# Kernel tuning notes

Measured on AMD Instinct MI355X. Metric: run time of the kernel, lower is better.

Reference implementation:

```python
import jax, jax.numpy as jnp
import numpy as np

S, N, CM, CZ, H, C = 256, 512, 256, 128, 8, 32
EPS = 1e-5


def layer_norm(x, gamma, beta):
    mu = jnp.mean(x, axis=-1, keepdims=True)
    var = jnp.var(x, axis=-1, keepdims=True)
    return (x - mu) * jax.lax.rsqrt(var + EPS) * gamma + beta


def setup_inputs() -> dict:
    key = jax.random.key(0)
    ks = jax.random.split(key, 10)
    sc = lambda fan_in: 1.0 / np.sqrt(fan_in)
    return {
        "msa_rep": jax.random.normal(ks[0], (S, N, CM), dtype=jnp.float32),
        "pair_rep": jax.random.normal(ks[1], (N, N, CZ), dtype=jnp.float32),
        "ln_msa_g": jnp.ones((CM,), jnp.float32),
        "ln_msa_b": jnp.zeros((CM,), jnp.float32),
        "Wv": jax.random.uniform(ks[2], (CM, H * C), jnp.float32, -sc(CM), sc(CM)),
        "bv": jax.random.uniform(ks[3], (H * C,), jnp.float32, -sc(CM), sc(CM)),
        "ln_z_g": jnp.ones((CZ,), jnp.float32),
        "ln_z_b": jnp.zeros((CZ,), jnp.float32),
        "Wb": jax.random.uniform(ks[4], (CZ, H), jnp.float32, -sc(CZ), sc(CZ)),
        "bb": jax.random.uniform(ks[5], (H,), jnp.float32, -sc(CZ), sc(CZ)),
        "Wg": jax.random.uniform(ks[6], (CM, H * C), jnp.float32, -sc(CM), sc(CM)),
        "bg": jax.random.uniform(ks[7], (H * C,), jnp.float32, -sc(CM), sc(CM)),
        "Wp": jax.random.uniform(ks[8], (H * C, CM), jnp.float32, -sc(H * C), sc(H * C)),
    }


def reference(msa_rep, pair_rep, ln_msa_g, ln_msa_b, Wv, bv, ln_z_g, ln_z_b, Wb, bb, Wg, bg, Wp):
    m = layer_norm(msa_rep, ln_msa_g, ln_msa_b)                 # [S,N,CM]
    v = (m @ Wv + bv).reshape(S, N, H, C)                       # [S,N,H,C]
    g = jax.nn.sigmoid(m @ Wg + bg).reshape(S, N, H, C)         # [S,N,H,C]
    b = layer_norm(pair_rep, ln_z_g, ln_z_b) @ Wb + bb          # [N,N,H]
    w = jax.nn.softmax(b, axis=-2)                              # softmax over key residue j
    # o[s,i,h,c] = sum_j w[i,j,h] * v[s,j,h,c]
    o = g * jnp.einsum('ijh,sjhc->sihc', w, v)                  # [S,N,H,C]
    return o.reshape(S, N, H * C) @ Wp                          # [S,N,CM]
```

## Files before the change

kernel.cpp:

```cpp
#include <hip/hip_runtime.h>
#include <hip/hip_bf16.h>
#include <math.h>

#define S 256
#define N 512
#define CM 256
#define CZ 128
#define H 8
#define C 32
#define HC 256

typedef __attribute__((ext_vector_type(8))) short short8v;
typedef __attribute__((ext_vector_type(4))) float f32x4;

#define GLOBAL_LOAD_LDS16(gsrc, ldst)                                          \
  __builtin_amdgcn_global_load_lds(                                            \
      (const __attribute__((address_space(1))) void*)(gsrc),                   \
      (__attribute__((address_space(3))) void*)(ldst), 16, 0, 0)

__global__ __launch_bounds__(256) void k_prep(
    const float* __restrict__ Wv, const float* __restrict__ Wg, const float* __restrict__ Wp,
    __hip_bfloat16* __restrict__ Wcat_t, __hip_bfloat16* __restrict__ Wp_t)
{
  const int k = blockIdx.x;
  const int n = threadIdx.x;
  Wcat_t[(size_t)n * CM + k]        = __float2bfloat16(Wv[(size_t)k * HC + n]);
  Wcat_t[(size_t)(n + HC) * CM + k] = __float2bfloat16(Wg[(size_t)k * HC + n]);
  Wp_t[(size_t)n * CM + k]          = __float2bfloat16(Wp[(size_t)k * CM + n]);
}

__global__ __launch_bounds__(256) void k_ln(
    const float* __restrict__ msa, const float* __restrict__ gamma, const float* __restrict__ beta,
    __hip_bfloat16* __restrict__ mbf)
{
  const int t = threadIdx.x, wav = t >> 6, lane = t & 63;
  const size_t row = (size_t)blockIdx.x * 4 + wav;
  const int k0 = lane * 4;
  const float4 xv = *(const float4*)(msa + row * CM + k0);
  float s  = xv.x + xv.y + xv.z + xv.w;
  float s2 = xv.x * xv.x + xv.y * xv.y + xv.z * xv.z + xv.w * xv.w;
#pragma unroll
  for (int off = 32; off > 0; off >>= 1) {
    s  += __shfl_xor(s, off);
    s2 += __shfl_xor(s2, off);
  }
  const float mu = s * (1.f / CM);
  const float rstd = rsqrtf(s2 * (1.f / CM) - mu * mu + 1e-5f);
  const float4 gm = *(const float4*)(gamma + k0);
  const float4 bt = *(const float4*)(beta + k0);
  union { __hip_bfloat16 b[4]; short4 v; } pk;
  pk.b[0] = __float2bfloat16((xv.x - mu) * rstd * gm.x + bt.x);
  pk.b[1] = __float2bfloat16((xv.y - mu) * rstd * gm.y + bt.y);
  pk.b[2] = __float2bfloat16((xv.z - mu) * rstd * gm.z + bt.z);
  pk.b[3] = __float2bfloat16((xv.w - mu) * rstd * gm.w + bt.w);
  *(short4*)(mbf + row * CM + k0) = pk.v;
}

__global__ __launch_bounds__(256) void k_mm1(
    const __hip_bfloat16* __restrict__ mbf, const __hip_bfloat16* __restrict__ Wcat_t,
    const float* __restrict__ bv, const float* __restrict__ bg,
    __hip_bfloat16* __restrict__ vc, __hip_bfloat16* __restrict__ gb)
{
  __shared__ __hip_bfloat16 Ac[2][8 * 128 * 8];
  __shared__ __hip_bfloat16 Bc[2][8 * 128 * 8];
  const int t = threadIdx.x;
  const int wave = t >> 6, lane = t & 63;
  const int wm = wave >> 1, wn = wave & 1;
  const int lr = lane & 15, lq = lane >> 4;
  const int n0 = blockIdx.x * 128;
  const int m0 = blockIdx.y * 128;
  const bool vhalf = (n0 < HC);

  f32x4 acc[4][4];
  if (vhalf) {
#pragma unroll
    for (int ni = 0; ni < 4; ++ni) {
      const float b_ = bv[n0 + wn * 64 + ni * 16 + lr];
#pragma unroll
      for (int mi = 0; mi < 4; ++mi) acc[mi][ni] = (f32x4)b_;
    }
  } else {
#pragma unroll
    for (int ni = 0; ni < 4; ++ni) {
      const float4 b4 = *(const float4*)&bg[(n0 - HC) + wn * 64 + ni * 16 + lq * 4];
#pragma unroll
      for (int mi = 0; mi < 4; ++mi) {
        acc[mi][ni][0] = b4.x; acc[mi][ni][1] = b4.y;
        acc[mi][ni][2] = b4.z; acc[mi][ni][3] = b4.w;
      }
    }
  }

  auto stage = [&](int p, int kt) {
#pragma unroll
    for (int u = 0; u < 2; ++u) {
      const int jb = wave * 2 + u;
#pragma unroll
      for (int ih = 0; ih < 2; ++ih) {
        GLOBAL_LOAD_LDS16(mbf + ((size_t)(m0 + ih * 64 + lane)) * CM + kt * 64 + jb * 8,
                          &Ac[p][(jb * 128 + ih * 64) * 8]);
        GLOBAL_LOAD_LDS16(Wcat_t + ((size_t)(n0 + ih * 64 + lane)) * CM + kt * 64 + jb * 8,
                          &Bc[p][(jb * 128 + ih * 64) * 8]);
      }
    }
  };

  stage(0, 0);
  __syncthreads();
  for (int kt = 0; kt < 4; ++kt) {
    const int p = kt & 1;
    if (kt < 3) stage(p ^ 1, kt + 1);
#pragma unroll
    for (int kh = 0; kh < 2; ++kh) {
      const int ldb = lq + kh * 4;
      short8v a[4], b[4];
#pragma unroll
      for (int mi = 0; mi < 4; ++mi)
        a[mi] = *(const short8v*)&Ac[p][((ldb * 128) + wm * 64 + mi * 16 + lr) * 8];
#pragma unroll
      for (int ni = 0; ni < 4; ++ni)
        b[ni] = *(const short8v*)&Bc[p][((ldb * 128) + wn * 64 + ni * 16 + lr) * 8];
      if (vhalf) {
#pragma unroll
        for (int mi = 0; mi < 4; ++mi)
#pragma unroll
          for (int ni = 0; ni < 4; ++ni)
            acc[mi][ni] = __builtin_amdgcn_mfma_f32_16x16x32_bf16(a[mi], b[ni], acc[mi][ni], 0, 0, 0);
      } else {
#pragma unroll
        for (int mi = 0; mi < 4; ++mi)
#pragma unroll
          for (int ni = 0; ni < 4; ++ni)
            acc[mi][ni] = __builtin_amdgcn_mfma_f32_16x16x32_bf16(b[ni], a[mi], acc[mi][ni], 0, 0, 0);
      }
    }
    __syncthreads();
  }

  if (vhalf) {
#pragma unroll
    for (int mi = 0; mi < 4; ++mi) {
      const int rowb = m0 + wm * 64 + mi * 16 + lq * 4;
      const int s = rowb >> 9;
      const int j = rowb & (N - 1);
      const int jb = j >> 3, jlo = (lq & 1) * 4;
#pragma unroll
      for (int ni = 0; ni < 4; ++ni) {
        const int col = n0 + wn * 64 + ni * 16 + lr;
        const int h = col >> 5, c = col & 31;
        union { __hip_bfloat16 b[4]; short4 v; } pk;
#pragma unroll
        for (int r = 0; r < 4; ++r) pk.b[r] = __float2bfloat16(acc[mi][ni][r]);
        *(short4*)(vc + ((size_t)(h * (N / 8) + jb) * (S * C) + s * C + c) * 8 + jlo) = pk.v;
      }
    }
  } else {
#pragma unroll
    for (int mi = 0; mi < 4; ++mi) {
      const int rowb = m0 + wm * 64 + mi * 16 + lr;
#pragma unroll
      for (int ni = 0; ni < 4; ++ni) {
        const int nb = (n0 - HC) + wn * 64 + ni * 16 + lq * 4;
        union { __hip_bfloat16 b[4]; short4 v; } pk;
#pragma unroll
        for (int r = 0; r < 4; ++r)
          pk.b[r] = __float2bfloat16(1.f / (1.f + __expf(-acc[mi][ni][r])));
        *(short4*)(gb + (size_t)rowb * HC + nb) = pk.v;
      }
    }
  }
}

__global__ __launch_bounds__(256) void k_ln_b(
    const float* __restrict__ pair, const float* __restrict__ gamma, const float* __restrict__ beta,
    const float* __restrict__ Wb, float* __restrict__ wbuf)
{
  const int t = threadIdx.x, wav = t >> 6, lane = t & 63;
  const int q = lane & 15, sub = lane >> 4;
  const int k0 = q * 8;

  float wreg[8][8];
#pragma unroll
  for (int kk = 0; kk < 8; ++kk) {
    *(float4*)&wreg[kk][0] = *(const float4*)&Wb[(k0 + kk) * H];
    *(float4*)&wreg[kk][4] = *(const float4*)&Wb[(k0 + kk) * H + 4];
  }
  const float4 gm0 = *(const float4*)(gamma + k0);
  const float4 gm1 = *(const float4*)(gamma + k0 + 4);
  const float4 bt0 = *(const float4*)(beta + k0);
  const float4 bt1 = *(const float4*)(beta + k0 + 4);

#pragma unroll 2
  for (int it = 0; it < 8; ++it) {
    const size_t row = (size_t)blockIdx.x * 128 + it * 16 + wav * 4 + sub;
    const float* x = pair + row * CZ + k0;
    const float4 x0 = *(const float4*)(x);
    const float4 x1 = *(const float4*)(x + 4);

    float s  = x0.x + x0.y + x0.z + x0.w + x1.x + x1.y + x1.z + x1.w;
    float s2 = x0.x * x0.x + x0.y * x0.y + x0.z * x0.z + x0.w * x0.w
             + x1.x * x1.x + x1.y * x1.y + x1.z * x1.z + x1.w * x1.w;
#pragma unroll
    for (int off = 8; off > 0; off >>= 1) {
      s  += __shfl_xor(s, off);
      s2 += __shfl_xor(s2, off);
    }
    const float mu = s * (1.f / CZ);
    const float rstd = rsqrtf(s2 * (1.f / CZ) - mu * mu + 1e-5f);

    float xn[8];
    xn[0] = (x0.x - mu) * rstd * gm0.x + bt0.x;
    xn[1] = (x0.y - mu) * rstd * gm0.y + bt0.y;
    xn[2] = (x0.z - mu) * rstd * gm0.z + bt0.z;
    xn[3] = (x0.w - mu) * rstd * gm0.w + bt0.w;
    xn[4] = (x1.x - mu) * rstd * gm1.x + bt1.x;
    xn[5] = (x1.y - mu) * rstd * gm1.y + bt1.y;
    xn[6] = (x1.z - mu) * rstd * gm1.z + bt1.z;
    xn[7] = (x1.w - mu) * rstd * gm1.w + bt1.w;

    float acc[8];
#pragma unroll
    for (int h = 0; h < 8; ++h) acc[h] = 0.f;
#pragma unroll
    for (int kk = 0; kk < 8; ++kk)
#pragma unroll
      for (int h = 0; h < 8; ++h) acc[h] += xn[kk] * wreg[kk][h];

#pragma unroll
    for (int h = 0; h < 8; ++h) {
#pragma unroll
      for (int off = 8; off > 0; off >>= 1) acc[h] += __shfl_xor(acc[h], off);
    }
    if (q == 0) {
      const size_t i = row >> 9;
      const size_t j = row & (N - 1);
#pragma unroll
      for (int h = 0; h < 8; ++h)
        wbuf[((size_t)h * N + i) * N + j] = acc[h];
    }
  }
}

__global__ __launch_bounds__(256) void k_softmax(
    const float* __restrict__ wbuf, __hip_bfloat16* __restrict__ wbh)
{
  const float* p = wbuf + (size_t)blockIdx.x * N;
  const int t = threadIdx.x, lane = t & 63, wav = t >> 6;
  float2 xv = *(const float2*)(p + t * 2);
  float mx = fmaxf(xv.x, xv.y);
#pragma unroll
  for (int off = 32; off > 0; off >>= 1) mx = fmaxf(mx, __shfl_xor(mx, off));
  __shared__ float redmax[4];
  __shared__ float redsum[4];
  if (lane == 0) redmax[wav] = mx;
  __syncthreads();
  mx = fmaxf(fmaxf(redmax[0], redmax[1]), fmaxf(redmax[2], redmax[3]));
  const float e0 = __expf(xv.x - mx), e1 = __expf(xv.y - mx);
  float sum = e0 + e1;
#pragma unroll
  for (int off = 32; off > 0; off >>= 1) sum += __shfl_xor(sum, off);
  if (lane == 0) redsum[wav] = sum;
  __syncthreads();
  sum = (redsum[0] + redsum[1]) + (redsum[2] + redsum[3]);
  const float inv = 1.f / sum;
  union { __hip_bfloat16 b[2]; int i; } pk;
  pk.b[0] = __float2bfloat16(e0 * inv);
  pk.b[1] = __float2bfloat16(e1 * inv);
  *(int*)((__hip_bfloat16*)(wbh + (size_t)blockIdx.x * N) + t * 2) = pk.i;
}

__global__ __launch_bounds__(256) void k_attn_mfma(
    const __hip_bfloat16* __restrict__ vc, const __hip_bfloat16* __restrict__ wbh,
    __hip_bfloat16* gb)
{
  __shared__ __hip_bfloat16 Ac[2][8 * 128 * 8];
  __shared__ __hip_bfloat16 Bc[2][8 * 128 * 8];

  const int t = threadIdx.x;
  const int wave = t >> 6, lane = t & 63;
  const int wm = wave >> 1, wn = wave & 1;
  const int lr = lane & 15, lq = lane >> 4;
  const int i0 = blockIdx.x * 128;
  const int n0 = blockIdx.y * 128;
  const int h  = blockIdx.z;

  f32x4 acc[4][4];
#pragma unroll
  for (int mi = 0; mi < 4; ++mi)
#pragma unroll
    for (int ni = 0; ni < 4; ++ni) acc[mi][ni] = (f32x4)0.f;

  const __hip_bfloat16* Abase = wbh + ((size_t)h * N + i0) * N;
  const __hip_bfloat16* Bbase = vc + (size_t)h * (N / 8) * (S * C) * 8 + (size_t)n0 * 8;

  auto stage = [&](int p, int kt) {
#pragma unroll
    for (int u = 0; u < 2; ++u) {
      const int jb = wave * 2 + u;
#pragma unroll
      for (int ih = 0; ih < 2; ++ih) {
        GLOBAL_LOAD_LDS16(Abase + ((size_t)(ih * 64 + lane)) * N + kt * 64 + jb * 8,
                          &Ac[p][(jb * 128 + ih * 64) * 8]);
        GLOBAL_LOAD_LDS16(Bbase + ((size_t)(kt * 8 + jb) * (S * C) + ih * 64 + lane) * 8,
                          &Bc[p][(jb * 128 + ih * 64) * 8]);
      }
    }
  };

  stage(0, 0);
  __syncthreads();
  for (int kt = 0; kt < 8; ++kt) {
    const int p = kt & 1;
    if (kt < 7) stage(p ^ 1, kt + 1);
#pragma unroll
    for (int kh = 0; kh < 2; ++kh) {
      const int ldb = lq + kh * 4;
      short8v a[4], b[4];
#pragma unroll
      for (int mi = 0; mi < 4; ++mi)
        a[mi] = *(const short8v*)&Ac[p][((ldb * 128) + wm * 64 + mi * 16 + lr) * 8];
#pragma unroll
      for (int ni = 0; ni < 4; ++ni)
        b[ni] = *(const short8v*)&Bc[p][((ldb * 128) + wn * 64 + ni * 16 + lr) * 8];
#pragma unroll
      for (int mi = 0; mi < 4; ++mi)
#pragma unroll
        for (int ni = 0; ni < 4; ++ni)
          acc[mi][ni] = __builtin_amdgcn_mfma_f32_16x16x32_bf16(b[ni], a[mi], acc[mi][ni], 0, 0, 0);
    }
    __syncthreads();
  }

#pragma unroll
  for (int mi = 0; mi < 4; ++mi) {
    const int i = i0 + wm * 64 + mi * 16 + lr;
#pragma unroll
    for (int ni = 0; ni < 4; ++ni) {
      const int nb = n0 + wn * 64 + ni * 16 + lq * 4;
      const int sidx = nb >> 5, c = nb & 31;
      __hip_bfloat16* gp = gb + (((size_t)sidx * N + i) << 8) + h * C + c;
      union { __hip_bfloat16 b[4]; short4 v; } gl, st;
      gl.v = *(const short4*)gp;
#pragma unroll
      for (int r = 0; r < 4; ++r)
        st.b[r] = __float2bfloat16(__bfloat162float(gl.b[r]) * acc[mi][ni][r]);
      *(short4*)gp = st.v;
    }
  }
}

__global__ __launch_bounds__(256) void k_out_mfma(
    const __hip_bfloat16* __restrict__ ogb, const __hip_bfloat16* __restrict__ Wp_t,
    float* __restrict__ out)
{
  __shared__ __hip_bfloat16 Ac[2][8 * 128 * 8];
  __shared__ __hip_bfloat16 Bc[2][8 * 128 * 8];
  const int t = threadIdx.x;
  const int wave = t >> 6, lane = t & 63;
  const int wm = wave >> 1, wn = wave & 1;
  const int lr = lane & 15, lq = lane >> 4;
  const int n0 = blockIdx.x * 128;
  const int m0 = blockIdx.y * 128;

  f32x4 acc[4][4];
#pragma unroll
  for (int mi = 0; mi < 4; ++mi)
#pragma unroll
    for (int ni = 0; ni < 4; ++ni) acc[mi][ni] = (f32x4)0.f;

  auto stage = [&](int p, int kt) {
#pragma unroll
    for (int u = 0; u < 2; ++u) {
      const int jb = wave * 2 + u;
#pragma unroll
      for (int ih = 0; ih < 2; ++ih) {
        GLOBAL_LOAD_LDS16(ogb + ((size_t)(m0 + ih * 64 + lane)) * CM + kt * 64 + jb * 8,
                          &Ac[p][(jb * 128 + ih * 64) * 8]);
        GLOBAL_LOAD_LDS16(Wp_t + ((size_t)(n0 + ih * 64 + lane)) * CM + kt * 64 + jb * 8,
                          &Bc[p][(jb * 128 + ih * 64) * 8]);
      }
    }
  };

  stage(0, 0);
  __syncthreads();
  for (int kt = 0; kt < 4; ++kt) {
    const int p = kt & 1;
    if (kt < 3) stage(p ^ 1, kt + 1);
#pragma unroll
    for (int kh = 0; kh < 2; ++kh) {
      const int ldb = lq + kh * 4;
      short8v a[4], b[4];
#pragma unroll
      for (int mi = 0; mi < 4; ++mi)
        a[mi] = *(const short8v*)&Ac[p][((ldb * 128) + wm * 64 + mi * 16 + lr) * 8];
#pragma unroll
      for (int ni = 0; ni < 4; ++ni)
        b[ni] = *(const short8v*)&Bc[p][((ldb * 128) + wn * 64 + ni * 16 + lr) * 8];
#pragma unroll
      for (int mi = 0; mi < 4; ++mi)
#pragma unroll
        for (int ni = 0; ni < 4; ++ni)
          acc[mi][ni] = __builtin_amdgcn_mfma_f32_16x16x32_bf16(a[mi], b[ni], acc[mi][ni], 0, 0, 0);
    }
    __syncthreads();
  }

#pragma unroll
  for (int mi = 0; mi < 4; ++mi) {
    const int rowb = m0 + wm * 64 + mi * 16 + lq * 4;
#pragma unroll
    for (int ni = 0; ni < 4; ++ni) {
      const int col = n0 + wn * 64 + ni * 16 + lr;
#pragma unroll
      for (int r = 0; r < 4; ++r)
        out[(size_t)(rowb + r) * CM + col] = acc[mi][ni][r];
    }
  }
}

extern "C" void kernel_launch(void* const* d_in, const int* in_sizes, int n_in,
                              void* d_out, int out_size, void* d_ws, size_t ws_size,
                              hipStream_t stream)
{
  const float* msa      = (const float*)d_in[0];
  const float* pair     = (const float*)d_in[1];
  const float* ln_msa_g = (const float*)d_in[2];
  const float* ln_msa_b = (const float*)d_in[3];
  const float* Wv       = (const float*)d_in[4];
  const float* bv       = (const float*)d_in[5];
  const float* ln_z_g   = (const float*)d_in[6];
  const float* ln_z_b   = (const float*)d_in[7];
  const float* Wb       = (const float*)d_in[8];
  const float* bb       = (const float*)d_in[9];
  const float* Wg       = (const float*)d_in[10];
  const float* bg       = (const float*)d_in[11];
  const float* Wp       = (const float*)d_in[12];
  float* out = (float*)d_out;
  (void)bb;

  char* w = (char*)d_ws;
  __hip_bfloat16* vc     = (__hip_bfloat16*)(w);
  __hip_bfloat16* mbf    = (__hip_bfloat16*)(w + 67108864);
  __hip_bfloat16* gb     = (__hip_bfloat16*)(w + 134217728);
  float*          wbuf   = (float*)         (w + 201326592);
  __hip_bfloat16* wbh    = (__hip_bfloat16*)(w + 209715200);
  __hip_bfloat16* Wcat_t = (__hip_bfloat16*)(w + 213909504);
  __hip_bfloat16* Wp_t   = (__hip_bfloat16*)(w + 214171648);

  k_prep<<<256, 256, 0, stream>>>(Wv, Wg, Wp, Wcat_t, Wp_t);
  k_ln<<<S * N / 4, 256, 0, stream>>>(msa, ln_msa_g, ln_msa_b, mbf);
  dim3 g1(4, S * N / 128);
  k_mm1<<<g1, 256, 0, stream>>>(mbf, Wcat_t, bv, bg, vc, gb);
  k_ln_b<<<N * N / 128, 256, 0, stream>>>(pair, ln_z_g, ln_z_b, Wb, wbuf);
  k_softmax<<<N * H, 256, 0, stream>>>(wbuf, wbh);
  dim3 g4(4, S * C / 128, H);
  k_attn_mfma<<<g4, 256, 0, stream>>>(vc, wbh, gb);
  dim3 g5(2, S * N / 128);
  k_out_mfma<<<g5, 256, 0, stream>>>(gb, Wp_t, out);
}
```

Baseline: 363.0 us.

## Single-buffer LDS in GEMM kernels and remap block IDs across XCDs

```diff
diff --git a/kernel.cpp b/kernel.cpp
--- a/kernel.cpp
+++ b/kernel.cpp
@@ -61,14 +61,16 @@
     const float* __restrict__ bv, const float* __restrict__ bg,
     __hip_bfloat16* __restrict__ vc, __hip_bfloat16* __restrict__ gb)
 {
-  __shared__ __hip_bfloat16 Ac[2][8 * 128 * 8];
-  __shared__ __hip_bfloat16 Bc[2][8 * 128 * 8];
+  __shared__ __hip_bfloat16 Ac[8 * 128 * 8];
+  __shared__ __hip_bfloat16 Bc[8 * 128 * 8];
   const int t = threadIdx.x;
   const int wave = t >> 6, lane = t & 63;
   const int wm = wave >> 1, wn = wave & 1;
   const int lr = lane & 15, lq = lane >> 4;
-  const int n0 = blockIdx.x * 128;
-  const int m0 = blockIdx.y * 128;
+  const int bid = blockIdx.x;
+  const int virt = (bid & 7) * 512 + (bid >> 3);
+  const int n0 = (virt & 3) * 128;
+  const int m0 = (virt >> 2) * 128;
   const bool vhalf = (n0 < HC);
 
   f32x4 acc[4][4];
@@ -91,35 +93,30 @@
     }
   }
 
-  auto stage = [&](int p, int kt) {
+  for (int kt = 0; kt < CM / 64; ++kt) {
+    __syncthreads();
 #pragma unroll
     for (int u = 0; u < 2; ++u) {
       const int jb = wave * 2 + u;
 #pragma unroll
       for (int ih = 0; ih < 2; ++ih) {
         GLOBAL_LOAD_LDS16(mbf + ((size_t)(m0 + ih * 64 + lane)) * CM + kt * 64 + jb * 8,
-                          &Ac[p][(jb * 128 + ih * 64) * 8]);
+                          &Ac[(jb * 128 + ih * 64) * 8]);
         GLOBAL_LOAD_LDS16(Wcat_t + ((size_t)(n0 + ih * 64 + lane)) * CM + kt * 64 + jb * 8,
-                          &Bc[p][(jb * 128 + ih * 64) * 8]);
-      }
-    }
-  };
-
-  stage(0, 0);
-  __syncthreads();
-  for (int kt = 0; kt < 4; ++kt) {
-    const int p = kt & 1;
-    if (kt < 3) stage(p ^ 1, kt + 1);
+                          &Bc[(jb * 128 + ih * 64) * 8]);
+      }
+    }
+    __syncthreads();
 #pragma unroll
     for (int kh = 0; kh < 2; ++kh) {
       const int ldb = lq + kh * 4;
       short8v a[4], b[4];
 #pragma unroll
       for (int mi = 0; mi < 4; ++mi)
-        a[mi] = *(const short8v*)&Ac[p][((ldb * 128) + wm * 64 + mi * 16 + lr) * 8];
+        a[mi] = *(const short8v*)&Ac[((ldb * 128) + wm * 64 + mi * 16 + lr) * 8];
 #pragma unroll
       for (int ni = 0; ni < 4; ++ni)
-        b[ni] = *(const short8v*)&Bc[p][((ldb * 128) + wn * 64 + ni * 16 + lr) * 8];
+        b[ni] = *(const short8v*)&Bc[((ldb * 128) + wn * 64 + ni * 16 + lr) * 8];
       if (vhalf) {
 #pragma unroll
         for (int mi = 0; mi < 4; ++mi)
@@ -134,7 +131,6 @@
             acc[mi][ni] = __builtin_amdgcn_mfma_f32_16x16x32_bf16(b[ni], a[mi], acc[mi][ni], 0, 0, 0);
       }
     }
-    __syncthreads();
   }
 
   if (vhalf) {
@@ -273,16 +269,18 @@
     const __hip_bfloat16* __restrict__ vc, const __hip_bfloat16* __restrict__ wbh,
     __hip_bfloat16* gb)
 {
-  __shared__ __hip_bfloat16 Ac[2][8 * 128 * 8];
-  __shared__ __hip_bfloat16 Bc[2][8 * 128 * 8];
+  __shared__ __hip_bfloat16 Ac[8 * 128 * 8];
+  __shared__ __hip_bfloat16 Bc[8 * 128 * 8];
 
   const int t = threadIdx.x;
   const int wave = t >> 6, lane = t & 63;
   const int wm = wave >> 1, wn = wave & 1;
   const int lr = lane & 15, lq = lane >> 4;
-  const int i0 = blockIdx.x * 128;
-  const int n0 = blockIdx.y * 128;
-  const int h  = blockIdx.z;
+  const int bid = blockIdx.x;
+  const int virt = (bid & 7) * 256 + (bid >> 3);
+  const int i0 = (virt & 3) * 128;
+  const int n0 = ((virt >> 2) & 63) * 128;
+  const int h  = virt >> 8;
 
   f32x4 acc[4][4];
 #pragma unroll
@@ -293,42 +291,37 @@
   const __hip_bfloat16* Abase = wbh + ((size_t)h * N + i0) * N;
   const __hip_bfloat16* Bbase = vc + (size_t)h * (N / 8) * (S * C) * 8 + (size_t)n0 * 8;
 
-  auto stage = [&](int p, int kt) {
+  for (int kt = 0; kt < N / 64; ++kt) {
+    __syncthreads();
 #pragma unroll
     for (int u = 0; u < 2; ++u) {
       const int jb = wave * 2 + u;
 #pragma unroll
       for (int ih = 0; ih < 2; ++ih) {
         GLOBAL_LOAD_LDS16(Abase + ((size_t)(ih * 64 + lane)) * N + kt * 64 + jb * 8,
-                          &Ac[p][(jb * 128 + ih * 64) * 8]);
+                          &Ac[(jb * 128 + ih * 64) * 8]);
         GLOBAL_LOAD_LDS16(Bbase + ((size_t)(kt * 8 + jb) * (S * C) + ih * 64 + lane) * 8,
-                          &Bc[p][(jb * 128 + ih * 64) * 8]);
-      }
-    }
-  };
-
-  stage(0, 0);
-  __syncthreads();
-  for (int kt = 0; kt < 8; ++kt) {
-    const int p = kt & 1;
-    if (kt < 7) stage(p ^ 1, kt + 1);
+                          &Bc[(jb * 128 + ih * 64) * 8]);
+      }
+    }
+    __syncthreads();
+
 #pragma unroll
     for (int kh = 0; kh < 2; ++kh) {
       const int ldb = lq + kh * 4;
       short8v a[4], b[4];
 #pragma unroll
       for (int mi = 0; mi < 4; ++mi)
-        a[mi] = *(const short8v*)&Ac[p][((ldb * 128) + wm * 64 + mi * 16 + lr) * 8];
+        a[mi] = *(const short8v*)&Ac[((ldb * 128) + wm * 64 + mi * 16 + lr) * 8];
 #pragma unroll
       for (int ni = 0; ni < 4; ++ni)
-        b[ni] = *(const short8v*)&Bc[p][((ldb * 128) + wn * 64 + ni * 16 + lr) * 8];
+        b[ni] = *(const short8v*)&Bc[((ldb * 128) + wn * 64 + ni * 16 + lr) * 8];
 #pragma unroll
       for (int mi = 0; mi < 4; ++mi)
 #pragma unroll
         for (int ni = 0; ni < 4; ++ni)
           acc[mi][ni] = __builtin_amdgcn_mfma_f32_16x16x32_bf16(b[ni], a[mi], acc[mi][ni], 0, 0, 0);
     }
-    __syncthreads();
   }
 
 #pragma unroll
@@ -353,14 +346,16 @@
     const __hip_bfloat16* __restrict__ ogb, const __hip_bfloat16* __restrict__ Wp_t,
     float* __restrict__ out)
 {
-  __shared__ __hip_bfloat16 Ac[2][8 * 128 * 8];
-  __shared__ __hip_bfloat16 Bc[2][8 * 128 * 8];
+  __shared__ __hip_bfloat16 Ac[8 * 128 * 8];
+  __shared__ __hip_bfloat16 Bc[8 * 128 * 8];
   const int t = threadIdx.x;
   const int wave = t >> 6, lane = t & 63;
   const int wm = wave >> 1, wn = wave & 1;
   const int lr = lane & 15, lq = lane >> 4;
-  const int n0 = blockIdx.x * 128;
-  const int m0 = blockIdx.y * 128;
+  const int bid = blockIdx.x;
+  const int virt = (bid & 7) * 256 + (bid >> 3);
+  const int n0 = (virt & 1) * 128;
+  const int m0 = (virt >> 1) * 128;
 
   f32x4 acc[4][4];
 #pragma unroll
@@ -368,42 +363,36 @@
 #pragma unroll
     for (int ni = 0; ni < 4; ++ni) acc[mi][ni] = (f32x4)0.f;
 
-  auto stage = [&](int p, int kt) {
+  for (int kt = 0; kt < CM / 64; ++kt) {
+    __syncthreads();
 #pragma unroll
     for (int u = 0; u < 2; ++u) {
       const int jb = wave * 2 + u;
 #pragma unroll
       for (int ih = 0; ih < 2; ++ih) {
         GLOBAL_LOAD_LDS16(ogb + ((size_t)(m0 + ih * 64 + lane)) * CM + kt * 64 + jb * 8,
-                          &Ac[p][(jb * 128 + ih * 64) * 8]);
+                          &Ac[(jb * 128 + ih * 64) * 8]);
         GLOBAL_LOAD_LDS16(Wp_t + ((size_t)(n0 + ih * 64 + lane)) * CM + kt * 64 + jb * 8,
-                          &Bc[p][(jb * 128 + ih * 64) * 8]);
-      }
-    }
-  };
-
-  stage(0, 0);
-  __syncthreads();
-  for (int kt = 0; kt < 4; ++kt) {
-    const int p = kt & 1;
-    if (kt < 3) stage(p ^ 1, kt + 1);
+                          &Bc[(jb * 128 + ih * 64) * 8]);
+      }
+    }
+    __syncthreads();
 #pragma unroll
     for (int kh = 0; kh < 2; ++kh) {
       const int ldb = lq + kh * 4;
       short8v a[4], b[4];
 #pragma unroll
       for (int mi = 0; mi < 4; ++mi)
-        a[mi] = *(const short8v*)&Ac[p][((ldb * 128) + wm * 64 + mi * 16 + lr) * 8];
+        a[mi] = *(const short8v*)&Ac[((ldb * 128) + wm * 64 + mi * 16 + lr) * 8];
 #pragma unroll
       for (int ni = 0; ni < 4; ++ni)
-        b[ni] = *(const short8v*)&Bc[p][((ldb * 128) + wn * 64 + ni * 16 + lr) * 8];
+        b[ni] = *(const short8v*)&Bc[((ldb * 128) + wn * 64 + ni * 16 + lr) * 8];
 #pragma unroll
       for (int mi = 0; mi < 4; ++mi)
 #pragma unroll
         for (int ni = 0; ni < 4; ++ni)
           acc[mi][ni] = __builtin_amdgcn_mfma_f32_16x16x32_bf16(a[mi], b[ni], acc[mi][ni], 0, 0, 0);
     }
-    __syncthreads();
   }
 
 #pragma unroll
@@ -450,12 +439,9 @@
 
   k_prep<<<256, 256, 0, stream>>>(Wv, Wg, Wp, Wcat_t, Wp_t);
   k_ln<<<S * N / 4, 256, 0, stream>>>(msa, ln_msa_g, ln_msa_b, mbf);
-  dim3 g1(4, S * N / 128);
-  k_mm1<<<g1, 256, 0, stream>>>(mbf, Wcat_t, bv, bg, vc, gb);
+  k_mm1<<<4096, 256, 0, stream>>>(mbf, Wcat_t, bv, bg, vc, gb);
   k_ln_b<<<N * N / 128, 256, 0, stream>>>(pair, ln_z_g, ln_z_b, Wb, wbuf);
   k_softmax<<<N * H, 256, 0, stream>>>(wbuf, wbh);
-  dim3 g4(4, S * C / 128, H);
-  k_attn_mfma<<<g4, 256, 0, stream>>>(vc, wbh, gb);
-  dim3 g5(2, S * N / 128);
-  k_out_mfma<<<g5, 256, 0, stream>>>(gb, Wp_t, out);
-}
+  k_attn_mfma<<<2048, 256, 0, stream>>>(vc, wbh, gb);
+  k_out_mfma<<<2048, 256, 0, stream>>>(gb, Wp_t, out);
+}
```

Result: no change. 356.3 us (-1.8%).
